# Optimization experiments

Measured on AMD Instinct MI355X. Metric: run time of the kernel, lower is better.

## Reference

```python
import jax, jax.numpy as jnp
import numpy as np

B, T, E, H = 4, 2048, 2048, 16
HD = E // H  # 128


def apply_rope(x, freqs):
    # x: (B, T, H, HD); freqs: (T, HD//2) rotation angles per position/pair
    cos = jnp.cos(freqs)[None, :, None, :]  # (1, T, 1, HD//2)
    sin = jnp.sin(freqs)[None, :, None, :]
    xr = x.reshape(*x.shape[:-1], HD // 2, 2)
    x1, x2 = xr[..., 0], xr[..., 1]
    out = jnp.stack([x1 * cos - x2 * sin, x1 * sin + x2 * cos], axis=-1)
    return out.reshape(x.shape)


def setup_inputs() -> dict:
    key = jax.random.key(0)
    k1, k2, k3, k4 = jax.random.split(key, 4)
    x = jax.random.normal(k1, (B, T, E), dtype=jnp.float32)
    freqs = jax.random.uniform(k2, (T, HD // 2), dtype=jnp.float32) * 6.28318
    w_qkv = jax.random.normal(k3, (3 * E, E), dtype=jnp.float32) * 0.02
    w_o = jax.random.normal(k4, (E, E), dtype=jnp.float32) * 0.02
    return {"x": x, "freqs": freqs, "w_qkv": w_qkv, "w_o": w_o}


def reference(x, freqs, w_qkv, w_o):
    b, t, e = x.shape
    qkv = x @ w_qkv.T                            # (B, T, 3E)
    qkv = qkv.reshape(b, t, 3, H, HD)
    q, k, v = qkv[:, :, 0], qkv[:, :, 1], qkv[:, :, 2]
    q = apply_rope(q, freqs)
    k = apply_rope(k, freqs)
    q = q.transpose(0, 2, 1, 3)                  # (B, H, T, HD)
    k = k.transpose(0, 2, 1, 3)
    v = v.transpose(0, 2, 1, 3)
    scale = 1.0 / np.sqrt(HD)
    scores = jnp.einsum('bhqd,bhkd->bhqk', q, k) * scale
    causal = jnp.tril(jnp.ones((t, t), dtype=bool))
    scores = jnp.where(causal[None, None], scores, jnp.finfo(scores.dtype).min)
    attn = jax.nn.softmax(scores, axis=-1)
    out = jnp.einsum('bhqk,bhkd->bhqd', attn, v)  # (B, H, T, HD)
    out = out.transpose(0, 2, 1, 3).reshape(b, t, e)
    return out @ w_o.T
```

## Files before the change

### kernel.cpp

```cpp
#include <hip/hip_runtime.h>
#include <type_traits>

#define DEV __device__ __forceinline__

typedef __attribute__((ext_vector_type(4))) float f32x4;
typedef __attribute__((ext_vector_type(8))) __bf16 bf16x8;
typedef __attribute__((ext_vector_type(8))) short s16x8;
typedef unsigned int u32;
typedef unsigned short u16;

DEV u16 f2bf(float f) {
  u32 u = __builtin_bit_cast(u32, f);
  u32 r = u + 0x7FFFu + ((u >> 16) & 1u);
  return (u16)(r >> 16);
}
DEV float bf2f(u16 h) {
  u32 u = ((u32)h) << 16;
  return __builtin_bit_cast(float, u);
}

template <typename A>
DEV auto mfma_sel(A a, A b, f32x4 c, int)
    -> decltype(__builtin_amdgcn_mfma_f32_16x16x32_bf16(a, b, c, 0, 0, 0)) {
  return __builtin_amdgcn_mfma_f32_16x16x32_bf16(a, b, c, 0, 0, 0);
}
template <typename A>
DEV f32x4 mfma_sel(A a, A b, f32x4 c, long) {
  using O = typename std::conditional<std::is_same<A, bf16x8>::value, s16x8, bf16x8>::type;
  return __builtin_amdgcn_mfma_f32_16x16x32_bf16(
      __builtin_bit_cast(O, a), __builtin_bit_cast(O, b), c, 0, 0, 0);
}
DEV f32x4 MFMA16(bf16x8 a, bf16x8 b, f32x4 c) { return mfma_sel(a, b, c, 0); }

DEV void gload_lds16(const void* g, void* l) {
  __builtin_amdgcn_global_load_lds(
      (__attribute__((address_space(1))) void*)(g),
      (__attribute__((address_space(3))) void*)(l), 16, 0, 0);
}

__global__ __launch_bounds__(256) void cvt_f32_bf16(const float* __restrict__ in,
                                                    u16* __restrict__ out, int n4) {
  int i = blockIdx.x * blockDim.x + threadIdx.x;
  const int stride = gridDim.x * blockDim.x;
  for (; i < n4; i += stride) {
    const float4 v = ((const float4*)in)[i];
    ushort4 o;
    o.x = f2bf(v.x); o.y = f2bf(v.y); o.z = f2bf(v.z); o.w = f2bf(v.w);
    ((ushort4*)out)[i] = o;
  }
}

__global__ __launch_bounds__(256) void build_cst(const float* __restrict__ freqs,
                                                 float2* __restrict__ cst, int n) {
  int i = blockIdx.x * blockDim.x + threadIdx.x;
  if (i < n) {
    float f = freqs[i];
    cst[i] = make_float2(cosf(f), sinf(f));
  }
}

template <int MODE>
__global__ __launch_bounds__(512, 2) void gemm_bt(const u16* __restrict__ A,
                                                  const u16* __restrict__ Bm,
                                                  void* __restrict__ Cp,
                                                  u16* __restrict__ q_r,
                                                  u16* __restrict__ k_r,
                                                  u16* __restrict__ v_r,
                                                  const float2* __restrict__ cst,
                                                  const int M, const int N, const int K) {
  __shared__ __align__(16) u16 As[4][256 * 32];
  __shared__ __align__(16) u16 Bs[4][256 * 32];
  const int tid = threadIdx.x;
  const int wid = tid >> 6;
  const int lane = tid & 63;
  const int lrow = lane & 15;
  const int lgrp = lane >> 4;

  const int gx = gridDim.x;
  const int nwg = gx * gridDim.y;
  int id = blockIdx.y * gx + blockIdx.x;
  const int cpx = nwg >> 3;
  id = (id & 7) * cpx + (id >> 3);
  const int row0 = (id / gx) * 256;
  const int col0 = (id % gx) * 256;

  const int wm = (wid >> 2) * 128;
  const int wn = (wid & 3) * 64;

  f32x4 acc[8][4] = {};

  const int sj0 = wid * 2;
  const int srow = lane >> 2;
  const int sc = lane & 3;

#define STAGE_HALF(SLOT, T, II)                                                   \
  do {                                                                            \
    const int j_ = sj0 + (II);                                                    \
    const int row_ = j_ * 16 + srow;                                              \
    const int ch_ = sc ^ ((row_ >> 1) & 3);                                       \
    const int k0_ = (T) * 32;                                                     \
    gload_lds16(A + (size_t)(row0 + row_) * K + k0_ + ch_ * 8,                    \
                (char*)&As[SLOT][0] + j_ * 1024);                                 \
    gload_lds16(Bm + (size_t)(col0 + row_) * K + k0_ + ch_ * 8,                   \
                (char*)&Bs[SLOT][0] + j_ * 1024);                                 \
  } while (0)

#define READS_B(SLOT)                                                             \
  _Pragma("unroll") for (int fn = 0; fn < 4; ++fn) {                              \
    const int brow_ = wn + fn * 16 + lrow;                                        \
    bfr[fn] = *(const bf16x8*)((const char*)&Bs[SLOT][0] + brow_ * 64 +           \
                               ((lgrp ^ ((brow_ >> 1) & 3)) << 4));               \
  }

#define READS_A(SLOT, QUAD)                                                       \
  _Pragma("unroll") for (int i_ = 0; i_ < 4; ++i_) {                              \
    const int arow_ = wm + ((QUAD) * 4 + i_) * 16 + lrow;                         \
    af[i_] = *(const bf16x8*)((const char*)&As[SLOT][0] + arow_ * 64 +            \
                              ((lgrp ^ ((arow_ >> 1) & 3)) << 4));                \
  }

#define MFMA_QUAD(QUAD)                                                           \
  __builtin_amdgcn_s_setprio(1);                                                  \
  _Pragma("unroll") for (int fm = 0; fm < 4; ++fm) {                              \
    _Pragma("unroll") for (int fn = 0; fn < 4; ++fn)                              \
      acc[(QUAD) * 4 + fm][fn] = MFMA16(af[fm], bfr[fn], acc[(QUAD) * 4 + fm][fn]); \
  }                                                                               \
  __builtin_amdgcn_s_setprio(0);

  const int nk = K >> 5;
  STAGE_HALF(0, 0, 0); STAGE_HALF(0, 0, 1);
  STAGE_HALF(1, 1, 0); STAGE_HALF(1, 1, 1);
  STAGE_HALF(2, 2, 0); STAGE_HALF(2, 2, 1);
  __builtin_amdgcn_sched_barrier(0);
  asm volatile("s_waitcnt vmcnt(8)" ::: "memory");
  __builtin_amdgcn_s_barrier();

  bf16x8 bfr[4], af[4];
  for (int t = 0; t < nk - 2; ++t) {
    const int slot = t & 3;
    const int ns = (t + 3) & 3;
    const bool dostage = (t + 3) < nk;
    READS_B(slot)
    READS_A(slot, 0)
    if (dostage) STAGE_HALF(ns, t + 3, 0);
    __builtin_amdgcn_sched_barrier(0);
    __builtin_amdgcn_s_barrier();
    MFMA_QUAD(0)
    __builtin_amdgcn_sched_barrier(0);
    __builtin_amdgcn_s_barrier();
    READS_A(slot, 1)
    if (dostage) STAGE_HALF(ns, t + 3, 1);
    __builtin_amdgcn_sched_barrier(0);
    __builtin_amdgcn_s_barrier();
    MFMA_QUAD(1)
    __builtin_amdgcn_sched_barrier(0);
    asm volatile("s_waitcnt vmcnt(8)" ::: "memory");
    __builtin_amdgcn_s_barrier();
  }
  {
    const int slot = (nk - 2) & 3;
    READS_B(slot) READS_A(slot, 0)
    __builtin_amdgcn_sched_barrier(0);
    __builtin_amdgcn_s_barrier();
    MFMA_QUAD(0)
    __builtin_amdgcn_s_barrier();
    READS_A(slot, 1)
    __builtin_amdgcn_sched_barrier(0);
    __builtin_amdgcn_s_barrier();
    MFMA_QUAD(1)
    __builtin_amdgcn_sched_barrier(0);
    asm volatile("s_waitcnt vmcnt(0)" ::: "memory");
    __builtin_amdgcn_s_barrier();
  }
  {
    const int slot = (nk - 1) & 3;
    READS_B(slot) READS_A(slot, 0)
    __builtin_amdgcn_sched_barrier(0);
    __builtin_amdgcn_s_barrier();
    MFMA_QUAD(0)
    __builtin_amdgcn_s_barrier();
    READS_A(slot, 1)
    MFMA_QUAD(1)
  }

  if constexpr (MODE == 0) {
    #pragma unroll
    for (int fm = 0; fm < 8; ++fm) {
      #pragma unroll
      for (int r = 0; r < 4; ++r) {
        const size_t rb = (size_t)(row0 + wm + fm * 16 + lgrp * 4 + r) * N + col0 + wn + lrow;
        #pragma unroll
        for (int fn = 0; fn < 4; ++fn)
          ((float*)Cp)[rb + fn * 16] = acc[fm][fn][r];
      }
    }
  } else {
    const int which = col0 >> 11;
    const int colw = (col0 & 2047) + wn;
    const int h = colw >> 7;
    const int d0 = colw & 127;
    u16* const dst0 = (which == 0) ? q_r : (which == 1) ? k_r : v_r;
    const bool isv = (which == 2);
    #pragma unroll
    for (int fm = 0; fm < 8; ++fm) {
      #pragma unroll
      for (int r = 0; r < 4; ++r) {
        const int grow = row0 + wm + fm * 16 + lgrp * 4 + r;
        const int bb = grow >> 11, tt = grow & 2047;
        u16* const drow = dst0 + (((size_t)(bb * 16 + h) * 2048 + tt) << 7);
        if (isv) {
          #pragma unroll
          for (int fn = 0; fn < 4; ++fn)
            drow[d0 + fn * 16 + lrow] = f2bf(acc[fm][fn][r]);
        } else {
          #pragma unroll
          for (int fn = 0; fn < 4; ++fn) {
            const float v = acc[fm][fn][r];
            const float p = __shfl_xor(v, 1);
            const int d = d0 + fn * 16 + lrow;
            const float2 cs = cst[tt * 64 + (d >> 1)];
            const float o = (lrow & 1) ? (p * cs.y + v * cs.x) : (v * cs.x - p * cs.y);
            drow[d] = f2bf(o);
          }
        }
      }
    }
  }
#undef STAGE_HALF
#undef READS_B
#undef READS_A
#undef MFMA_QUAD
}

__global__ __launch_bounds__(256) void vtrans(const u16* __restrict__ vr,
                                              u16* __restrict__ vt) {
  constexpr int T = 2048;
  __shared__ u16 tile[64][130];
  const int t0 = blockIdx.x * 64;
  const int bh = blockIdx.y;
  const int tid = threadIdx.x;
  {
    const int tl = tid >> 2;
    const int cg = (tid & 3) * 32;
    const u16* src = vr + ((size_t)bh * T + t0 + tl) * 128 + cg;
    #pragma unroll
    for (int jj = 0; jj < 32; ++jj)
      tile[tl][cg + jj] = src[jj];
  }
  __syncthreads();
  {
    const int d = tid >> 1, half = tid & 1;
    u16* dst = vt + ((size_t)bh * 128 + d) * T + t0 + half * 32;
    #pragma unroll
    for (int jj = 0; jj < 32; ++jj)
      dst[jj] = tile[half * 32 + jj][d];
  }
}

__global__ __launch_bounds__(512, 2) void attn_fwd(const u16* __restrict__ Qp,
                                                   const u16* __restrict__ Kp,
                                                   const u16* __restrict__ Vp,
                                                   u16* __restrict__ Op) {
  constexpr int T = 2048;
  __shared__ __align__(16) u16 Kl[4][64 * 128];
  __shared__ __align__(16) u16 Vl[4][128 * 64];
  __shared__ __align__(16) u16 Pl[8 * 1024];

  const int tid = threadIdx.x;
  const int wid = tid >> 6;
  const int lane = tid & 63;
  const int lrow = lane & 15;
  const int lgrp = lane >> 4;

  const int lin = blockIdx.y * 4 + blockIdx.x;
  const int qa = lin >> 6;
  const int bh = ((lin & 7) << 3) | ((lin >> 3) & 7);

  const u16* Qb = Qp + (size_t)bh * T * 128;
  const u16* Kb = Kp + (size_t)bh * T * 128;
  const u16* Vb = Vp + (size_t)bh * 128 * T;

  const float CE = 0.08838834765f * 1.44269504089f;
  const float DTH = 12.0f / CE;
  const int s0 = (lane & 48) + ((lane & 48) >> 2);
  char* Pw = (char*)Pl + wid * 2048;
  const int ob = bh >> 4, oh = bh & 15;

  auto stage = [&](int buf, int kv0) {
    #pragma unroll
    for (int ii = 0; ii < 2; ++ii) {
      const int i = wid * 2 + ii;
      {
        const int rr = i * 4 + (lane >> 4);
        const int cs = (lane & 15) ^ (rr & 7);
        gload_lds16(Kb + (size_t)(kv0 + rr) * 128 + cs * 8, (char*)&Kl[buf][0] + i * 1024);
      }
      {
        const int rr = i * 8 + (lane >> 3);
        const int cs = (lane & 7) ^ (rr & 7);
        gload_lds16(Vb + (size_t)rr * T + kv0 + cs * 8, (char*)&Vl[buf][0] + i * 1024);
      }
    }
  };

  auto process = [&](const int qi) {
    const int q0 = qi * 256;
    const int wq0 = q0 + wid * 32;

    bf16x8 qf[2][4];
    #pragma unroll
    for (int qg = 0; qg < 2; ++qg) {
      const int qrow = wq0 + qg * 16 + lrow;
      #pragma unroll
      for (int db = 0; db < 4; ++db)
        qf[qg][db] = *(const bf16x8*)(Qb + (size_t)qrow * 128 + db * 32 + lgrp * 8);
    }

    f32x4 o[2][8] = {};
    float m[2] = {-3e38f, -3e38f};
    float l[2] = {0.f, 0.f};

    const int nkv = 4 * qi + 4;
    stage(0, 0);
    stage(1, 64);
    stage(2, 128);
    for (int j = 0; j < nkv; ++j) {
      if (j <= nkv - 3)      asm volatile("s_waitcnt vmcnt(8)" ::: "memory");
      else if (j == nkv - 2) asm volatile("s_waitcnt vmcnt(4)" ::: "memory");
      else                   asm volatile("s_waitcnt vmcnt(0)" ::: "memory");
      __builtin_amdgcn_s_barrier();
      if (j + 3 < nkv) stage((j + 3) & 3, (j + 3) * 64);
      const int cs = j & 3;
      const int kv0 = j * 64;

      if (kv0 <= wq0 + 31) {
        f32x4 s[2][4] = {};
        #pragma unroll
        for (int t4 = 0; t4 < 4; ++t4) {
          const int krow = t4 * 16 + lrow;
          #pragma unroll
          for (int db = 0; db < 4; ++db) {
            const int ch = (db * 4 + lgrp) ^ (krow & 7);
            bf16x8 kf = *(const bf16x8*)((const char*)&Kl[cs][0] + krow * 256 + ch * 16);
            s[0][t4] = MFMA16(kf, qf[0][db], s[0][t4]);
            s[1][t4] = MFMA16(kf, qf[1][db], s[1][t4]);
          }
        }

        if (kv0 + 63 > wq0) {
          #pragma unroll
          for (int qg = 0; qg < 2; ++qg) {
            const int lim = wq0 + qg * 16 + lrow - kv0 - lgrp * 4;
            #pragma unroll
            for (int t4 = 0; t4 < 4; ++t4) {
              #pragma unroll
              for (int r = 0; r < 4; ++r)
                if (t4 * 16 + r > lim) s[qg][t4][r] = -3e38f;
            }
          }
        }

        float pmax[2];
        #pragma unroll
        for (int qg = 0; qg < 2; ++qg) {
          float pm = fmaxf(fmaxf(s[qg][0][0], s[qg][0][1]), fmaxf(s[qg][0][2], s[qg][0][3]));
          #pragma unroll
          for (int t4 = 1; t4 < 4; ++t4)
            pm = fmaxf(pm, fmaxf(fmaxf(s[qg][t4][0], s[qg][t4][1]),
                                 fmaxf(s[qg][t4][2], s[qg][t4][3])));
          pm = fmaxf(pm, __shfl_xor(pm, 16));
          pm = fmaxf(pm, __shfl_xor(pm, 32));
          pmax[qg] = pm;
        }

        float alpha[2] = {1.f, 1.f};
        const float dmax = fmaxf(pmax[0] - m[0], pmax[1] - m[1]);
        if (__any(dmax > DTH)) {
          #pragma unroll
          for (int qg = 0; qg < 2; ++qg) {
            const float mn = fmaxf(m[qg], pmax[qg]);
            alpha[qg] = exp2f((m[qg] - mn) * CE);
            m[qg] = mn;
          }
          #pragma unroll
          for (int qg = 0; qg < 2; ++qg) {
            #pragma unroll
            for (int r = 0; r < 4; ++r) {
              const float a4 = __shfl(alpha[qg], s0 + r);
              #pragma unroll
              for (int db = 0; db < 8; ++db)
                o[qg][db][r] *= a4;
            }
          }
        }

        #pragma unroll
        for (int qg = 0; qg < 2; ++qg) {
          float psum = 0.f;
          #pragma unroll
          for (int t4 = 0; t4 < 4; ++t4) {
            #pragma unroll
            for (int r = 0; r < 4; ++r) {
              const float p = exp2f((s[qg][t4][r] - m[qg]) * CE);
              s[qg][t4][r] = p;
              psum += p;
            }
          }
          psum += __shfl_xor(psum, 16);
          psum += __shfl_xor(psum, 32);
          l[qg] = l[qg] * alpha[qg] + psum;

          #pragma unroll
          for (int t4 = 0; t4 < 4; ++t4) {
            uint2 w;
            w.x = (u32)f2bf(s[qg][t4][0]) | ((u32)f2bf(s[qg][t4][1]) << 16);
            w.y = (u32)f2bf(s[qg][t4][2]) | ((u32)f2bf(s[qg][t4][3]) << 16);
            const int off = lrow * 128 + (((t4 * 2 + (lgrp >> 1)) ^ (lrow & 7)) << 4) + (lgrp & 1) * 8;
            *(uint2*)(Pw + off) = w;
          }
          asm volatile("s_waitcnt lgkmcnt(0)" ::: "memory");
          __builtin_amdgcn_sched_barrier(0);

          bf16x8 pa[2];
          #pragma unroll
          for (int kb = 0; kb < 2; ++kb)
            pa[kb] = *(const bf16x8*)(Pw + lrow * 128 + (((kb * 4 + lgrp) ^ (lrow & 7)) << 4));
          #pragma unroll
          for (int db = 0; db < 8; ++db) {
            const int vrow = db * 16 + lrow;
            #pragma unroll
            for (int kb = 0; kb < 2; ++kb) {
              const int vch = (kb * 4 + lgrp) ^ (vrow & 7);
              bf16x8 vf = *(const bf16x8*)((const char*)&Vl[cs][0] + vrow * 128 + vch * 16);
              o[qg][db] = MFMA16(pa[kb], vf, o[qg][db]);
            }
          }
        }
      }
    }

    #pragma unroll
    for (int qg = 0; qg < 2; ++qg) {
      const float inv = 1.f / l[qg];
      float inv4[4];
      #pragma unroll
      for (int r = 0; r < 4; ++r) inv4[r] = __shfl(inv, s0 + r);
      #pragma unroll
      for (int db = 0; db < 8; ++db) {
        #pragma unroll
        for (int r = 0; r < 4; ++r) {
          const int qrow = wq0 + qg * 16 + lgrp * 4 + r;
          Op[((size_t)ob * T + qrow) * 2048 + oh * 128 + db * 16 + lrow] =
              f2bf(o[qg][db][r] * inv4[r]);
        }
      }
    }
  };

  process(7 - qa);
  __syncthreads();
  process(qa);
}

extern "C" void kernel_launch(void* const* d_in, const int* in_sizes, int n_in,
                              void* d_out, int out_size, void* d_ws, size_t ws_size,
                              hipStream_t stream) {
  const float* x = (const float*)d_in[0];
  const float* freqs = (const float*)d_in[1];
  const float* w_qkv = (const float*)d_in[2];
  const float* w_o = (const float*)d_in[3];

  constexpr int B = 4, T = 2048, E = 2048, H = 16;
  constexpr size_t M = (size_t)B * T;
  constexpr int N3 = 3 * E;

  char* ws = (char*)d_ws;
  size_t off = 0;
  auto alloc = [&](size_t bytes) {
    void* p = ws + off;
    off += (bytes + 255) & ~(size_t)255;
    return p;
  };
  u16* wqkv_bf = (u16*)alloc((size_t)N3 * E * 2);
  u16* wo_bf   = (u16*)alloc((size_t)E * E * 2);
  u16* x_bf    = (u16*)alloc(M * E * 2);
  u16* q_r     = (u16*)alloc(M * E * 2);
  u16* k_r     = (u16*)alloc(M * E * 2);
  u16* v_r     = (u16*)alloc(M * E * 2);
  u16* vt      = (u16*)alloc(M * E * 2);
  u16* attn_o  = (u16*)alloc(M * E * 2);
  float2* cst  = (float2*)alloc((size_t)T * 64 * 8);

  cvt_f32_bf16<<<2048, 256, 0, stream>>>(x, x_bf, (int)(M * E / 4));
  cvt_f32_bf16<<<2048, 256, 0, stream>>>(w_qkv, wqkv_bf, N3 * E / 4);
  cvt_f32_bf16<<<2048, 256, 0, stream>>>(w_o, wo_bf, E * E / 4);
  build_cst<<<(T * 64) / 256, 256, 0, stream>>>(freqs, cst, T * 64);

  gemm_bt<2><<<dim3(N3 / 256, (int)(M / 256)), 512, 0, stream>>>(
      x_bf, wqkv_bf, nullptr, q_r, k_r, v_r, cst, (int)M, N3, E);
  vtrans<<<dim3(T / 64, B * H), 256, 0, stream>>>(v_r, vt);
  attn_fwd<<<dim3(4, B * H), 512, 0, stream>>>(q_r, k_r, vt, attn_o);
  gemm_bt<0><<<dim3(E / 256, (int)(M / 256)), 512, 0, stream>>>(
      attn_o, wo_bf, d_out, nullptr, nullptr, nullptr, nullptr, (int)M, E, E);
}
```

Baseline: 465.8 us.

## Collapse GEMM main loop to one barrier per k-step with unified tail

```diff
diff --git a/kernel.cpp b/kernel.cpp
--- a/kernel.cpp
+++ b/kernel.cpp
@@ -131,54 +131,22 @@
   STAGE_HALF(0, 0, 0); STAGE_HALF(0, 0, 1);
   STAGE_HALF(1, 1, 0); STAGE_HALF(1, 1, 1);
   STAGE_HALF(2, 2, 0); STAGE_HALF(2, 2, 1);
-  __builtin_amdgcn_sched_barrier(0);
-  asm volatile("s_waitcnt vmcnt(8)" ::: "memory");
-  __builtin_amdgcn_s_barrier();
 
   bf16x8 bfr[4], af[4];
-  for (int t = 0; t < nk - 2; ++t) {
+  for (int t = 0; t < nk; ++t) {
     const int slot = t & 3;
     const int ns = (t + 3) & 3;
     const bool dostage = (t + 3) < nk;
+    if (t <= nk - 3)      asm volatile("s_waitcnt vmcnt(8)" ::: "memory");
+    else if (t == nk - 2) asm volatile("s_waitcnt vmcnt(4)" ::: "memory");
+    else                  asm volatile("s_waitcnt vmcnt(0)" ::: "memory");
+    __builtin_amdgcn_s_barrier();
+    __builtin_amdgcn_sched_barrier(0);
+    if (dostage) STAGE_HALF(ns, t + 3, 0);
     READS_B(slot)
     READS_A(slot, 0)
-    if (dostage) STAGE_HALF(ns, t + 3, 0);
-    __builtin_amdgcn_sched_barrier(0);
-    __builtin_amdgcn_s_barrier();
     MFMA_QUAD(0)
-    __builtin_amdgcn_sched_barrier(0);
-    __builtin_amdgcn_s_barrier();
-    READS_A(slot, 1)
     if (dostage) STAGE_HALF(ns, t + 3, 1);
-    __builtin_amdgcn_sched_barrier(0);
-    __builtin_amdgcn_s_barrier();
-    MFMA_QUAD(1)
-    __builtin_amdgcn_sched_barrier(0);
-    asm volatile("s_waitcnt vmcnt(8)" ::: "memory");
-    __builtin_amdgcn_s_barrier();
-  }
-  {
-    const int slot = (nk - 2) & 3;
-    READS_B(slot) READS_A(slot, 0)
-    __builtin_amdgcn_sched_barrier(0);
-    __builtin_amdgcn_s_barrier();
-    MFMA_QUAD(0)
-    __builtin_amdgcn_s_barrier();
-    READS_A(slot, 1)
-    __builtin_amdgcn_sched_barrier(0);
-    __builtin_amdgcn_s_barrier();
-    MFMA_QUAD(1)
-    __builtin_amdgcn_sched_barrier(0);
-    asm volatile("s_waitcnt vmcnt(0)" ::: "memory");
-    __builtin_amdgcn_s_barrier();
-  }
-  {
-    const int slot = (nk - 1) & 3;
-    READS_B(slot) READS_A(slot, 0)
-    __builtin_amdgcn_sched_barrier(0);
-    __builtin_amdgcn_s_barrier();
-    MFMA_QUAD(0)
-    __builtin_amdgcn_s_barrier();
     READS_A(slot, 1)
     MFMA_QUAD(1)
   }
```

After: 516.9 us. 1.11x slower.

## Fold softmax scale into Q, cut KV ring to three stages, share V loads across query groups

Applied to the files above, without the earlier changes.

```diff
diff --git a/kernel.cpp b/kernel.cpp
--- a/kernel.cpp
+++ b/kernel.cpp
@@ -201,6 +201,7 @@
     const int d0 = colw & 127;
     u16* const dst0 = (which == 0) ? q_r : (which == 1) ? k_r : v_r;
     const bool isv = (which == 2);
+    const float wscale = (which == 0) ? (0.08838834765f * 1.44269504089f) : 1.0f;
     #pragma unroll
     for (int fm = 0; fm < 8; ++fm) {
       #pragma unroll
@@ -219,7 +220,7 @@
             const float p = __shfl_xor(v, 1);
             const int d = d0 + fn * 16 + lrow;
             const float2 cs = cst[tt * 64 + (d >> 1)];
-            const float o = (lrow & 1) ? (p * cs.y + v * cs.x) : (v * cs.x - p * cs.y);
+            const float o = ((lrow & 1) ? (p * cs.y + v * cs.x) : (v * cs.x - p * cs.y)) * wscale;
             drow[d] = f2bf(o);
           }
         }
@@ -262,9 +263,9 @@
                                                    const u16* __restrict__ Vp,
                                                    u16* __restrict__ Op) {
   constexpr int T = 2048;
-  __shared__ __align__(16) u16 Kl[4][64 * 128];
-  __shared__ __align__(16) u16 Vl[4][128 * 64];
-  __shared__ __align__(16) u16 Pl[8 * 1024];
+  __shared__ __align__(16) u16 Kl[3][64 * 128];
+  __shared__ __align__(16) u16 Vl[3][128 * 64];
+  __shared__ __align__(16) u16 Pl[8 * 2048];
 
   const int tid = threadIdx.x;
   const int wid = tid >> 6;
@@ -280,10 +281,9 @@
   const u16* Kb = Kp + (size_t)bh * T * 128;
   const u16* Vb = Vp + (size_t)bh * 128 * T;
 
-  const float CE = 0.08838834765f * 1.44269504089f;
-  const float DTH = 12.0f / CE;
+  const float DTH = 12.0f;
   const int s0 = (lane & 48) + ((lane & 48) >> 2);
-  char* Pw = (char*)Pl + wid * 2048;
+  char* Pw = (char*)Pl + wid * 4096;
   const int ob = bh >> 4, oh = bh & 15;
 
   auto stage = [&](int buf, int kv0) {
@@ -323,29 +323,32 @@
     const int nkv = 4 * qi + 4;
     stage(0, 0);
     stage(1, 64);
-    stage(2, 128);
+    int csl = 0;
     for (int j = 0; j < nkv; ++j) {
-      if (j <= nkv - 3)      asm volatile("s_waitcnt vmcnt(8)" ::: "memory");
-      else if (j == nkv - 2) asm volatile("s_waitcnt vmcnt(4)" ::: "memory");
-      else                   asm volatile("s_waitcnt vmcnt(0)" ::: "memory");
+      if (j < nkv - 1) asm volatile("s_waitcnt vmcnt(4)" ::: "memory");
+      else             asm volatile("s_waitcnt vmcnt(0)" ::: "memory");
       __builtin_amdgcn_s_barrier();
-      if (j + 3 < nkv) stage((j + 3) & 3, (j + 3) * 64);
-      const int cs = j & 3;
+      if (j + 2 < nkv) {
+        int ss = csl + 2; if (ss >= 3) ss -= 3;
+        stage(ss, (j + 2) * 64);
+      }
       const int kv0 = j * 64;
 
       if (kv0 <= wq0 + 31) {
         f32x4 s[2][4] = {};
+        __builtin_amdgcn_s_setprio(1);
         #pragma unroll
         for (int t4 = 0; t4 < 4; ++t4) {
           const int krow = t4 * 16 + lrow;
           #pragma unroll
           for (int db = 0; db < 4; ++db) {
             const int ch = (db * 4 + lgrp) ^ (krow & 7);
-            bf16x8 kf = *(const bf16x8*)((const char*)&Kl[cs][0] + krow * 256 + ch * 16);
+            bf16x8 kf = *(const bf16x8*)((const char*)&Kl[csl][0] + krow * 256 + ch * 16);
             s[0][t4] = MFMA16(kf, qf[0][db], s[0][t4]);
             s[1][t4] = MFMA16(kf, qf[1][db], s[1][t4]);
           }
         }
+        __builtin_amdgcn_s_setprio(0);
 
         if (kv0 + 63 > wq0) {
           #pragma unroll
@@ -379,7 +382,7 @@
           #pragma unroll
           for (int qg = 0; qg < 2; ++qg) {
             const float mn = fmaxf(m[qg], pmax[qg]);
-            alpha[qg] = exp2f((m[qg] - mn) * CE);
+            alpha[qg] = exp2f(m[qg] - mn);
             m[qg] = mn;
           }
           #pragma unroll
@@ -394,49 +397,60 @@
           }
         }
 
+        float psum[2] = {0.f, 0.f};
         #pragma unroll
         for (int qg = 0; qg < 2; ++qg) {
-          float psum = 0.f;
           #pragma unroll
           for (int t4 = 0; t4 < 4; ++t4) {
             #pragma unroll
             for (int r = 0; r < 4; ++r) {
-              const float p = exp2f((s[qg][t4][r] - m[qg]) * CE);
+              const float p = exp2f(s[qg][t4][r] - m[qg]);
               s[qg][t4][r] = p;
-              psum += p;
+              psum[qg] += p;
             }
           }
-          psum += __shfl_xor(psum, 16);
-          psum += __shfl_xor(psum, 32);
-          l[qg] = l[qg] * alpha[qg] + psum;
-
+          psum[qg] += __shfl_xor(psum[qg], 16);
+          psum[qg] += __shfl_xor(psum[qg], 32);
+          l[qg] = l[qg] * alpha[qg] + psum[qg];
+        }
+
+        #pragma unroll
+        for (int qg = 0; qg < 2; ++qg) {
           #pragma unroll
           for (int t4 = 0; t4 < 4; ++t4) {
             uint2 w;
             w.x = (u32)f2bf(s[qg][t4][0]) | ((u32)f2bf(s[qg][t4][1]) << 16);
             w.y = (u32)f2bf(s[qg][t4][2]) | ((u32)f2bf(s[qg][t4][3]) << 16);
             const int off = lrow * 128 + (((t4 * 2 + (lgrp >> 1)) ^ (lrow & 7)) << 4) + (lgrp & 1) * 8;
-            *(uint2*)(Pw + off) = w;
-          }
-          asm volatile("s_waitcnt lgkmcnt(0)" ::: "memory");
-          __builtin_amdgcn_sched_barrier(0);
-
-          bf16x8 pa[2];
+            *(uint2*)(Pw + qg * 2048 + off) = w;
+          }
+        }
+        asm volatile("s_waitcnt lgkmcnt(0)" ::: "memory");
+        __builtin_amdgcn_sched_barrier(0);
+
+        bf16x8 pa[2][2];
+        #pragma unroll
+        for (int qg = 0; qg < 2; ++qg) {
           #pragma unroll
           for (int kb = 0; kb < 2; ++kb)
-            pa[kb] = *(const bf16x8*)(Pw + lrow * 128 + (((kb * 4 + lgrp) ^ (lrow & 7)) << 4));
-          #pragma unroll
-          for (int db = 0; db < 8; ++db) {
-            const int vrow = db * 16 + lrow;
-            #pragma unroll
-            for (int kb = 0; kb < 2; ++kb) {
-              const int vch = (kb * 4 + lgrp) ^ (vrow & 7);
-              bf16x8 vf = *(const bf16x8*)((const char*)&Vl[cs][0] + vrow * 128 + vch * 16);
-              o[qg][db] = MFMA16(pa[kb], vf, o[qg][db]);
-            }
-          }
-        }
-      }
+            pa[qg][kb] = *(const bf16x8*)(Pw + qg * 2048 + lrow * 128 +
+                                          (((kb * 4 + lgrp) ^ (lrow & 7)) << 4));
+        }
+        __builtin_amdgcn_s_setprio(1);
+        #pragma unroll
+        for (int db = 0; db < 8; ++db) {
+          const int vrow = db * 16 + lrow;
+          #pragma unroll
+          for (int kb = 0; kb < 2; ++kb) {
+            const int vch = (kb * 4 + lgrp) ^ (vrow & 7);
+            bf16x8 vf = *(const bf16x8*)((const char*)&Vl[csl][0] + vrow * 128 + vch * 16);
+            o[0][db] = MFMA16(pa[0][kb], vf, o[0][db]);
+            o[1][db] = MFMA16(pa[1][kb], vf, o[1][db]);
+          }
+        }
+        __builtin_amdgcn_s_setprio(0);
+      }
+      csl = (csl == 2) ? 0 : csl + 1;
     }
 
     #pragma unroll
```

Measured after the change: 463.5 us. Within noise of the previous version (-0.5%).
